# Performance work log

Measured on AMD Instinct MI355X. Metric: run time of the kernel, lower is better.

The kernel has to match this reference:

```python
import jax, jax.numpy as jnp
import numpy as np

B, N, I, H, O, E, HD = 4, 2048, 32, 64, 32, 2, 2  # batch, nodes, in_dim, hidden, out, edgetypes, heads
D1 = H * HD * E  # layer-1 filter input dim (concat of all heads/edgetypes from layer 0)


def setup_inputs() -> dict:
    key = jax.random.key(0)
    ks = jax.random.split(key, 20)
    s = 0.1
    return {
        "nodes": jax.random.normal(ks[0], (B, N, I), jnp.float32),
        "edges": jax.random.normal(ks[1], (B, N, N, E), jnp.float32),
        "W_emb": jax.random.normal(ks[2], (I, H), jnp.float32) * s,
        "b_emb": jnp.zeros((H,), jnp.float32),
        "Wf0": jax.random.normal(ks[3], (E, HD, H, H), jnp.float32) * s,
        "w1_0": jax.random.normal(ks[4], (E, HD, H), jnp.float32) * s,
        "b1_0": jnp.zeros((E, HD), jnp.float32),
        "w2_0": jax.random.normal(ks[5], (E, HD, H), jnp.float32) * s,
        "b2_0": jnp.zeros((E, HD), jnp.float32),
        "bias0": jax.random.normal(ks[6], (HD, H), jnp.float32) * s,  # state_bias aliased across edgetypes (list-mult bug)
        "Wf1": jax.random.normal(ks[7], (E, HD, D1, H), jnp.float32) * s,
        "w1_1": jax.random.normal(ks[8], (E, HD, H), jnp.float32) * s,
        "b1_1": jnp.zeros((E, HD), jnp.float32),
        "w2_1": jax.random.normal(ks[9], (E, HD, H), jnp.float32) * s,
        "b2_1": jnp.zeros((E, HD), jnp.float32),
        "bias1": jax.random.normal(ks[10], (HD, H), jnp.float32) * s,
        "W_out": jax.random.normal(ks[11], (H, O), jnp.float32) * s,
        "b_out": jnp.zeros((O,), jnp.float32),
    }


def _gat_layer(state, Wf, w1, b1, w2, b2, bias, edges_t, last):
    # state: (B,N,Din); Wf: (E,HD,Din,H); edges_t: (E,B,N,N)
    Wh = jnp.einsum('bnd,ehdk->ehbnk', state, Wf)                     # (E,HD,B,N,H)
    a1 = jnp.einsum('ehbnk,ehk->ehbn', Wh, w1) + b1[:, :, None, None]
    a2 = jnp.einsum('ehbnk,ehk->ehbn', Wh, w2) + b2[:, :, None, None]
    logits = jax.nn.leaky_relu(a1[..., :, None] + a2[..., None, :], 0.2) + edges_t[:, None]
    att = jax.nn.softmax(logits, axis=-2)                             # torch softmax dim=1 (over rows)
    msg = jnp.einsum('ehbik,ehbkd->ehbid', att, Wh) + bias[None, :, None, None, :]
    if last:
        return jnp.mean(jax.nn.elu(msg), axis=(0, 1))                 # (B,N,H)
    # concat in (edgetype-major, head-minor) order, matching the python loops
    return jnp.transpose(msg, (2, 3, 0, 1, 4)).reshape(msg.shape[2], msg.shape[3], -1)


def reference(nodes, edges, W_emb, b_emb, Wf0, w1_0, b1_0, w2_0, b2_0, bias0,
              Wf1, w1_1, b1_1, w2_1, b2_1, bias1, W_out, b_out):
    edges_t = jnp.transpose(edges, (3, 0, 1, 2))                      # (E,B,N,N)
    state = nodes @ W_emb + b_emb                                     # embedding
    state = _gat_layer(state, Wf0, w1_0, b1_0, w2_0, b2_0, bias0, edges_t, last=False)
    state = _gat_layer(state, Wf1, w1_1, b1_1, w2_1, b2_1, bias1, edges_t, last=True)
    out = state @ W_out + b_out                                       # (B,N,O)
    return jnp.mean(out, axis=1)                                      # graph-level output (B,O)
```

## Files before the change

### kernel.cpp

```cpp
#include <hip/hip_runtime.h>
#include <hip/hip_bf16.h>


constexpr int B_  = 4;
constexpr int N_  = 2048;
constexpr int I_  = 32;
constexpr int H_  = 64;
constexpr int O_  = 32;
constexpr int EH_ = 4;
constexpr int D1_ = 256;
constexpr int BN_ = B_ * N_;
constexpr int NC_ = 64;
constexpr int CH_ = N_ / NC_;
constexpr int TI_ = 16;
constexpr int TK_ = 32;
constexpr int NKT_ = N_ / TK_;

typedef __bf16 bf16x8 __attribute__((ext_vector_type(8)));
typedef float floatx4 __attribute__((ext_vector_type(4)));

constexpr float L2E_ = 1.4426950408889634f;

__device__ __forceinline__ unsigned short f2b(float f) {
    unsigned int u = __float_as_uint(f);
    return (unsigned short)((u + 0x7fffu + ((u >> 16) & 1u)) >> 16);
}

__device__ __forceinline__ float fexp2(float x) {
#if __has_builtin(__builtin_amdgcn_exp2f)
    return __builtin_amdgcn_exp2f(x);
#else
    return __expf(x * 0.6931471805599453f);
#endif
}

__global__ __launch_bounds__(256) void prep_kernel(
        const float* __restrict__ nodes, const float* __restrict__ W_emb,
        const float* __restrict__ b_emb, const float* __restrict__ Wf0,
        const float* __restrict__ Wf1, unsigned short* __restrict__ state0B,
        unsigned short* __restrict__ WfB0, unsigned short* __restrict__ WfB1) {
    int blk = blockIdx.x;
    int t = threadIdx.x;
    __shared__ float sn[4][I_];
    if (blk < 2048) {
        int r = t >> 6, h = t & 63;
        if (t < 4 * I_) {
            int rr = t / I_, ii = t % I_;
            sn[rr][ii] = nodes[(size_t)(blk * 4 + rr) * I_ + ii];
        }
        __syncthreads();
        float acc = b_emb[h];
        #pragma unroll
        for (int i = 0; i < I_; ++i) acc += sn[r][i] * W_emb[i * H_ + h];
        state0B[(size_t)(blk * 4 + r) * H_ + h] = f2b(acc);
    } else if (blk < 2048 + 64) {
        int o = (blk - 2048) * 256 + t;
        int k = o & 63, n = (o >> 6) & 63, c = o >> 12;
        WfB0[o] = f2b(Wf0[((size_t)c * 64 + k) * 64 + n]);
    } else {
        int o = (blk - 2112) * 256 + t;
        int k = o & 255, n = (o >> 8) & 63, c = o >> 14;
        WfB1[o] = f2b(Wf1[((size_t)c * 256 + k) * 64 + n]);
    }
}

template <int DIN>
__global__ __launch_bounds__(256) void wh_a_mfma_kernel(
        const unsigned short* __restrict__ stateB, const unsigned short* __restrict__ WfB,
        const float* __restrict__ w1, const float* __restrict__ b1,
        const float* __restrict__ w2, const float* __restrict__ b2,
        unsigned short* __restrict__ WhB, float* __restrict__ a1,
        float* __restrict__ a2) {
    int t = threadIdx.x;
    int lane = t & 63, wv = t >> 6;
    int col = lane & 15, qd = lane >> 4;
    int bn0 = blockIdx.x * TI_;
    int b = bn0 >> 11;

    floatx4 acc[4] = {{0,0,0,0},{0,0,0,0},{0,0,0,0},{0,0,0,0}};
    const unsigned short* __restrict__ ap = stateB + (size_t)(bn0 + col) * DIN + qd * 8;
    const unsigned short* __restrict__ bp = WfB + ((size_t)(wv * 64 + col) * DIN + qd * 8);
    #pragma unroll
    for (int k0 = 0; k0 < DIN; k0 += 32) {
        bf16x8 af = *(const bf16x8*)(ap + k0);
        #pragma unroll
        for (int nt = 0; nt < 4; ++nt) {
            bf16x8 bf = *(const bf16x8*)(bp + (size_t)nt * 16 * DIN + k0);
            acc[nt] = __builtin_amdgcn_mfma_f32_16x16x32_bf16(af, bf, acc[nt], 0, 0, 0);
        }
    }
    int nb = ((bn0 & 2047) >> 3) + (qd >> 1);
    #pragma unroll
    for (int nt = 0; nt < 4; ++nt) {
        unsigned int lo = (unsigned int)f2b(acc[nt][0]) | ((unsigned int)f2b(acc[nt][1]) << 16);
        unsigned int hi = (unsigned int)f2b(acc[nt][2]) | ((unsigned int)f2b(acc[nt][3]) << 16);
        uint2 v = make_uint2(lo, hi);
        *(uint2*)(WhB + ((((size_t)(wv * B_ + b) * 256 + nb) * 64 + nt * 16 + col) * 8
                         + (qd & 1) * 4)) = v;
    }
    float p1[4] = {}, p2[4] = {};
    #pragma unroll
    for (int nt = 0; nt < 4; ++nt) {
        float w1n = w1[wv * H_ + nt * 16 + col];
        float w2n = w2[wv * H_ + nt * 16 + col];
        #pragma unroll
        for (int r = 0; r < 4; ++r) {
            p1[r] += acc[nt][r] * w1n;
            p2[r] += acc[nt][r] * w2n;
        }
    }
    #pragma unroll
    for (int m = 1; m < 16; m <<= 1)
        #pragma unroll
        for (int r = 0; r < 4; ++r) {
            p1[r] += __shfl_xor(p1[r], m, 64);
            p2[r] += __shfl_xor(p2[r], m, 64);
        }
    if (col == 0) {
        float b1c = b1[wv], b2c = b2[wv];
        #pragma unroll
        for (int r = 0; r < 4; ++r) {
            a1[(size_t)wv * BN_ + bn0 + qd * 4 + r] = (p1[r] + b1c) * L2E_;
            a2[(size_t)wv * BN_ + bn0 + qd * 4 + r] = (p2[r] + b2c) * L2E_;
        }
    }
}

__global__ __launch_bounds__(256) void stats_kernel(
        const float* __restrict__ edges, const float* __restrict__ a1,
        const float* __restrict__ a2, float* __restrict__ ps) {
    int blk = blockIdx.x;
    int jt = blk & 7;
    int ic = (blk >> 3) & (NC_ - 1);
    int b  = blk >> 9;
    int t = threadIdx.x;
    int j = jt * 256 + t;
    __shared__ float sa1[EH_][CH_];
    for (int q = t; q < EH_ * CH_; q += 256) {
        int cc = q / CH_, ii = q % CH_;
        sa1[cc][ii] = a1[(size_t)cc * BN_ + b * N_ + ic * CH_ + ii];
    }
    __syncthreads();
    float a2v[EH_], s[EH_];
    #pragma unroll
    for (int cc = 0; cc < EH_; ++cc) {
        a2v[cc] = a2[(size_t)cc * BN_ + b * N_ + j];
        s[cc] = 0.f;
    }
    const float2* __restrict__ ep = (const float2*)edges + ((size_t)(b * N_ + ic * CH_)) * N_ + j;
    #pragma unroll 4
    for (int ii = 0; ii < CH_; ++ii) {
        float2 u = ep[(size_t)ii * N_];
        #pragma unroll
        for (int cc = 0; cc < EH_; ++cc) {
            float x = sa1[cc][ii] + a2v[cc];
            float l = fmaxf(x, 0.2f * x);
            s[cc] += fexp2(fmaf((cc < 2) ? u.x : u.y, L2E_, l));
        }
    }
    #pragma unroll
    for (int cc = 0; cc < EH_; ++cc)
        ps[((size_t)ic * EH_ + cc) * BN_ + b * N_ + j] = s[cc];
}

__global__ __launch_bounds__(256) void scale_kernel(
        const float* __restrict__ ps, unsigned short* __restrict__ WhB) {
    int t = threadIdx.x;
    int m0 = blockIdx.x * 256;
    int cb = m0 >> 14;
    int c = cb >> 2, b = cb & 3;
    int k0 = ((m0 >> 6) & 255) * 8;
    __shared__ float sD[32];
    if (t < 32) {
        float S = 0.f;
        const float* pp = ps + (size_t)c * BN_ + b * N_ + k0 + t;
        #pragma unroll 8
        for (int ic = 0; ic < NC_; ++ic) S += pp[(size_t)ic * EH_ * BN_];
        sD[t] = 1.f / S;
    }
    __syncthreads();
    unsigned short* wp = WhB + (size_t)(m0 + t) * 8;
    uint4 w = *(const uint4*)wp;
    int nbo = (t >> 6) * 8;
    unsigned int words[4] = {w.x, w.y, w.z, w.w};
    #pragma unroll
    for (int q = 0; q < 4; ++q) {
        float lo = __uint_as_float((words[q] & 0xffffu) << 16) * sD[nbo + 2 * q];
        float hi = __uint_as_float(words[q] & 0xffff0000u) * sD[nbo + 2 * q + 1];
        words[q] = (unsigned)f2b(lo) | ((unsigned)f2b(hi) << 16);
    }
    *(uint4*)wp = make_uint4(words[0], words[1], words[2], words[3]);
}

template <int LAST>
__global__ __launch_bounds__(512, 4) void mac_kernel(
        const float* __restrict__ edges, const float* __restrict__ a1,
        const float* __restrict__ a2s, const unsigned short* __restrict__ WhB,
        const float* __restrict__ bias, void* __restrict__ outv) {
    int t = threadIdx.x;
    int blk = blockIdx.x;
    int b = blk >> 7;
    int i0 = (blk & 127) * TI_;
    int lane = t & 63, wv = t >> 6;
    int c  = wv & 3;
    int kh = wv >> 2;
    int col = lane & 15;
    int qd  = lane >> 4;
    int esel = c >> 1;

    __shared__ float sa2[EH_][N_];
    __shared__ float sred[EH_][TI_][H_ + 1];

    for (int q = t; q < EH_ * (N_ / 4); q += 512) {
        int cc = q >> 9, kk = q & 511;
        ((float4*)sa2[cc])[kk] =
            ((const float4*)(a2s + (size_t)cc * BN_ + b * N_))[kk];
    }

    float a1v = a1[(size_t)c * BN_ + b * N_ + i0 + col];
    const float* __restrict__ erow = edges + (size_t)(b * N_ + i0 + col) * (N_ * 2);
    const unsigned short* __restrict__ whb0 = WhB + (size_t)(c * B_ + b) * (256 * 512);

    const int kt0 = kh * (NKT_ / 2);
    const int ktEnd = kt0 + NKT_ / 2;

    float evc[8], evn[8];
    {
        const float4* ep = (const float4*)(erow + (size_t)(kt0 * TK_ + qd * 8) * 2);
        #pragma unroll
        for (int jj = 0; jj < 4; ++jj) {
            float4 v = ep[jj];
            evc[2 * jj]     = esel ? v.y : v.x;
            evc[2 * jj + 1] = esel ? v.w : v.z;
        }
    }
    bf16x8 bcur[4], bnxt[4];
    #pragma unroll
    for (int nt = 0; nt < 4; ++nt)
        bcur[nt] = *(const bf16x8*)(whb0 + ((size_t)(kt0 * 4 + qd) * 64 + nt * 16 + col) * 8);

    floatx4 acc[4] = {{0,0,0,0},{0,0,0,0},{0,0,0,0},{0,0,0,0}};
    __syncthreads();

    for (int kt = kt0; kt < ktEnd; ++kt) {
        int ktn = (kt + 1 < ktEnd) ? (kt + 1) : kt0;
        {
            const float4* ep = (const float4*)(erow + (size_t)(ktn * TK_ + qd * 8) * 2);
            #pragma unroll
            for (int jj = 0; jj < 4; ++jj) {
                float4 v = ep[jj];
                evn[2 * jj]     = esel ? v.y : v.x;
                evn[2 * jj + 1] = esel ? v.w : v.z;
            }
        }
        #pragma unroll
        for (int nt = 0; nt < 4; ++nt)
            bnxt[nt] = *(const bf16x8*)(whb0 + ((size_t)(ktn * 4 + qd) * 64 + nt * 16 + col) * 8);

        const float4* sp = (const float4*)&sa2[c][kt * TK_ + qd * 8];
        float4 s0 = sp[0], s1 = sp[1];
        float az[8] = {s0.x, s0.y, s0.z, s0.w, s1.x, s1.y, s1.z, s1.w};
        bf16x8 af;
        #pragma unroll
        for (int j = 0; j < 8; ++j) {
            float sx = a1v + az[j];
            float u  = fmaxf(sx, 0.2f * sx);
            af[j] = (__bf16)fexp2(fmaf(evc[j], L2E_, u));
        }
        #pragma unroll
        for (int nt = 0; nt < 4; ++nt)
            acc[nt] = __builtin_amdgcn_mfma_f32_16x16x32_bf16(af, bcur[nt], acc[nt], 0, 0, 0);
        #pragma unroll
        for (int nt = 0; nt < 4; ++nt) bcur[nt] = bnxt[nt];
        #pragma unroll
        for (int j = 0; j < 8; ++j) evc[j] = evn[j];
    }

    if (kh == 1) {
        #pragma unroll
        for (int nt = 0; nt < 4; ++nt)
            #pragma unroll
            for (int r = 0; r < 4; ++r)
                sred[c][qd * 4 + r][nt * 16 + col] = acc[nt][r];
    }
    __syncthreads();
    if (kh == 0) {
        if (LAST) {
            #pragma unroll
            for (int nt = 0; nt < 4; ++nt) {
                float bb = bias[(c & 1) * H_ + nt * 16 + col];
                #pragma unroll
                for (int r = 0; r < 4; ++r) {
                    float x = acc[nt][r] + sred[c][qd * 4 + r][nt * 16 + col] + bb;
                    sred[c][qd * 4 + r][nt * 16 + col] =
                        x > 0.f ? x : (__expf(x) - 1.f);
                }
            }
        } else {
            unsigned short* out = (unsigned short*)outv;
            #pragma unroll
            for (int nt = 0; nt < 4; ++nt) {
                float bb = bias[(c & 1) * H_ + nt * 16 + col];
                #pragma unroll
                for (int r = 0; r < 4; ++r) {
                    float x = acc[nt][r] + sred[c][qd * 4 + r][nt * 16 + col] + bb;
                    out[((size_t)(b * N_ + i0 + qd * 4 + r)) * D1_ + c * H_ + nt * 16 + col]
                        = f2b(x);
                }
            }
        }
    }
    if (LAST) {
        __syncthreads();
        if (t < 64) {
            float s = 0.f;
            #pragma unroll
            for (int r = 0; r < TI_; ++r)
                s += sred[0][r][t] + sred[1][r][t] + sred[2][r][t] + sred[3][r][t];
            ((float*)outv)[(size_t)blk * 64 + t] = s * 0.25f;
        }
    }
}

__global__ __launch_bounds__(256) void out_kernel(
        const float* __restrict__ po, const float* __restrict__ W_out,
        const float* __restrict__ b_out, float* __restrict__ out) {
    int b = blockIdx.x, t = threadIdx.x;
    int d = t & 63, g0 = t >> 6;
    float s = 0.f;
    for (int g = g0; g < 128; g += 4) s += po[(size_t)(b * 128 + g) * 64 + d];
    __shared__ float red[4][H_];
    red[g0][d] = s;
    __syncthreads();
    if (t < H_) red[0][t] = (red[0][t] + red[1][t] + red[2][t] + red[3][t]) * (1.f / N_);
    __syncthreads();
    if (t < O_) {
        float acc = b_out[t];
        #pragma unroll 8
        for (int dd = 0; dd < H_; ++dd)
            acc += red[0][dd] * W_out[dd * O_ + t];
        out[b * O_ + t] = acc;
    }
}

extern "C" void kernel_launch(void* const* d_in, const int* in_sizes, int n_in,
                              void* d_out, int out_size, void* d_ws, size_t ws_size,
                              hipStream_t stream) {
    const float* nodes = (const float*)d_in[0];
    const float* edges = (const float*)d_in[1];
    const float* W_emb = (const float*)d_in[2];
    const float* b_emb = (const float*)d_in[3];
    const float* Wf0   = (const float*)d_in[4];
    const float* w1_0  = (const float*)d_in[5];
    const float* b1_0  = (const float*)d_in[6];
    const float* w2_0  = (const float*)d_in[7];
    const float* b2_0  = (const float*)d_in[8];
    const float* bias0 = (const float*)d_in[9];
    const float* Wf1   = (const float*)d_in[10];
    const float* w1_1  = (const float*)d_in[11];
    const float* b1_1  = (const float*)d_in[12];
    const float* w2_1  = (const float*)d_in[13];
    const float* b2_1  = (const float*)d_in[14];
    const float* bias1 = (const float*)d_in[15];
    const float* W_out = (const float*)d_in[16];
    const float* b_out = (const float*)d_in[17];

    float* ws = (float*)d_ws;
    unsigned short* state0B = (unsigned short*)ws;
    unsigned short* state1B = (unsigned short*)(ws + 262144);
    unsigned short* WhB  = (unsigned short*)(ws + 262144 + 1048576);
    unsigned short* WfB0 = (unsigned short*)(ws + 2359296);
    unsigned short* WfB1 = (unsigned short*)(ws + 2367488);
    float* a1 = ws + 2400256;
    float* a2 = ws + 2433024;
    float* ps = ws + 2465792;
    float* po = ws + 4562944;

    prep_kernel<<<2368, 256, 0, stream>>>(nodes, W_emb, b_emb, Wf0, Wf1,
                                          state0B, WfB0, WfB1);

    wh_a_mfma_kernel<H_><<<BN_ / TI_, 256, 0, stream>>>(state0B, WfB0, w1_0, b1_0,
                                                        w2_0, b2_0, WhB, a1, a2);
    stats_kernel<<<B_ * NC_ * (N_ / 256), 256, 0, stream>>>(edges, a1, a2, ps);
    scale_kernel<<<1024, 256, 0, stream>>>(ps, WhB);
    mac_kernel<0><<<B_ * (N_ / TI_), 512, 0, stream>>>(edges, a1, a2, WhB, bias0, state1B);
    wh_a_mfma_kernel<D1_><<<BN_ / TI_, 256, 0, stream>>>(state1B, WfB1, w1_1, b1_1,
                                                         w2_1, b2_1, WhB, a1, a2);
    stats_kernel<<<B_ * NC_ * (N_ / 256), 256, 0, stream>>>(edges, a1, a2, ps);
    scale_kernel<<<1024, 256, 0, stream>>>(ps, WhB);
    mac_kernel<1><<<B_ * (N_ / TI_), 512, 0, stream>>>(edges, a1, a2, WhB, bias1, po);

    out_kernel<<<B_, 256, 0, stream>>>(po, W_out, b_out, (float*)d_out);
}
```

Baseline: 438.5 us.

## Split mac kernel across channel pairs with 4-way K split, widen stats loads

The mac kernel now launches twice as many blocks. Each block handles two of the four edgetype/head channels and splits the K range four ways across waves, reducing partials through shared memory. It drops the register double-buffered prefetch and raises the occupancy hint. The stats kernel has each thread process two columns with float4 edge loads, and out_kernel is adapted to the new partial layout. The aim is more parallelism and smaller shared memory per block for better occupancy, but each block now reads the edges rows for only one edge type, so edge traffic in the mac kernel doubles.

```diff
diff --git a/kernel.cpp b/kernel.cpp
--- a/kernel.cpp
+++ b/kernel.cpp
@@ -130,37 +130,46 @@
         const float* __restrict__ edges, const float* __restrict__ a1,
         const float* __restrict__ a2, float* __restrict__ ps) {
     int blk = blockIdx.x;
-    int jt = blk & 7;
-    int ic = (blk >> 3) & (NC_ - 1);
-    int b  = blk >> 9;
+    int jt = blk & 3;
+    int ic = (blk >> 2) & (NC_ - 1);
+    int b  = blk >> 8;
     int t = threadIdx.x;
-    int j = jt * 256 + t;
+    int j0 = jt * 512 + t * 2;
     __shared__ float sa1[EH_][CH_];
-    for (int q = t; q < EH_ * CH_; q += 256) {
-        int cc = q / CH_, ii = q % CH_;
+    if (t < EH_ * CH_) {
+        int cc = t >> 5, ii = t & 31;
         sa1[cc][ii] = a1[(size_t)cc * BN_ + b * N_ + ic * CH_ + ii];
     }
     __syncthreads();
-    float a2v[EH_], s[EH_];
+    float a2x[EH_], a2y[EH_], s0[EH_], s1[EH_];
     #pragma unroll
     for (int cc = 0; cc < EH_; ++cc) {
-        a2v[cc] = a2[(size_t)cc * BN_ + b * N_ + j];
-        s[cc] = 0.f;
-    }
-    const float2* __restrict__ ep = (const float2*)edges + ((size_t)(b * N_ + ic * CH_)) * N_ + j;
+        float2 av = *(const float2*)(a2 + (size_t)cc * BN_ + b * N_ + j0);
+        a2x[cc] = av.x; a2y[cc] = av.y;
+        s0[cc] = 0.f; s1[cc] = 0.f;
+    }
+    const float4* __restrict__ ep =
+        (const float4*)edges + (((size_t)(b * N_ + ic * CH_) * N_ + j0) >> 1);
     #pragma unroll 4
     for (int ii = 0; ii < CH_; ++ii) {
-        float2 u = ep[(size_t)ii * N_];
+        float4 u = ep[(size_t)ii * (N_ >> 1)];
         #pragma unroll
         for (int cc = 0; cc < EH_; ++cc) {
-            float x = sa1[cc][ii] + a2v[cc];
-            float l = fmaxf(x, 0.2f * x);
-            s[cc] += fexp2(fmaf((cc < 2) ? u.x : u.y, L2E_, l));
+            float base = sa1[cc][ii];
+            float xa = base + a2x[cc];
+            float xb = base + a2y[cc];
+            float la = fmaxf(xa, 0.2f * xa);
+            float lb = fmaxf(xb, 0.2f * xb);
+            float ea = (cc < 2) ? u.x : u.y;
+            float eb = (cc < 2) ? u.z : u.w;
+            s0[cc] += fexp2(fmaf(ea, L2E_, la));
+            s1[cc] += fexp2(fmaf(eb, L2E_, lb));
         }
     }
     #pragma unroll
     for (int cc = 0; cc < EH_; ++cc)
-        ps[((size_t)ic * EH_ + cc) * BN_ + b * N_ + j] = s[cc];
+        *(float2*)&ps[((size_t)ic * EH_ + cc) * BN_ + b * N_ + j0] =
+            make_float2(s0[cc], s1[cc]);
 }
 
 __global__ __launch_bounds__(256) void scale_kernel(
@@ -193,106 +202,114 @@
 }
 
 template <int LAST>
-__global__ __launch_bounds__(512, 4) void mac_kernel(
+__global__ __launch_bounds__(512, 8) void mac_kernel(
         const float* __restrict__ edges, const float* __restrict__ a1,
         const float* __restrict__ a2s, const unsigned short* __restrict__ WhB,
         const float* __restrict__ bias, void* __restrict__ outv) {
     int t = threadIdx.x;
     int blk = blockIdx.x;
-    int b = blk >> 7;
-    int i0 = (blk & 127) * TI_;
+    int cp = blk & 1;
+    int g  = blk >> 1;
+    int b  = g >> 7;
+    int i0 = (g & 127) * TI_;
     int lane = t & 63, wv = t >> 6;
-    int c  = wv & 3;
-    int kh = wv >> 2;
+    int kq = wv >> 1;
+    int cl = wv & 1;
+    int c  = cp * 2 + cl;
     int col = lane & 15;
     int qd  = lane >> 4;
-    int esel = c >> 1;
-
-    __shared__ float sa2[EH_][N_];
-    __shared__ float sred[EH_][TI_][H_ + 1];
-
-    for (int q = t; q < EH_ * (N_ / 4); q += 512) {
-        int cc = q >> 9, kk = q & 511;
-        ((float4*)sa2[cc])[kk] =
-            ((const float4*)(a2s + (size_t)cc * BN_ + b * N_))[kk];
+
+    __shared__ float sa2[2][N_];
+    __shared__ float sA[2][TI_][H_ + 1];
+    __shared__ float sB[2][TI_][H_ + 1];
+
+    for (int q = t; q < 2 * (N_ / 4); q += 512) {
+        int cl_ = q >> 9, kk = q & 511;
+        ((float4*)sa2[cl_])[kk] =
+            ((const float4*)(a2s + (size_t)(cp * 2 + cl_) * BN_ + b * N_))[kk];
     }
 
     float a1v = a1[(size_t)c * BN_ + b * N_ + i0 + col];
     const float* __restrict__ erow = edges + (size_t)(b * N_ + i0 + col) * (N_ * 2);
-    const unsigned short* __restrict__ whb0 = WhB + (size_t)(c * B_ + b) * (256 * 512);
-
-    const int kt0 = kh * (NKT_ / 2);
-    const int ktEnd = kt0 + NKT_ / 2;
-
-    float evc[8], evn[8];
-    {
-        const float4* ep = (const float4*)(erow + (size_t)(kt0 * TK_ + qd * 8) * 2);
-        #pragma unroll
-        for (int jj = 0; jj < 4; ++jj) {
-            float4 v = ep[jj];
-            evc[2 * jj]     = esel ? v.y : v.x;
-            evc[2 * jj + 1] = esel ? v.w : v.z;
-        }
-    }
-    bf16x8 bcur[4], bnxt[4];
-    #pragma unroll
-    for (int nt = 0; nt < 4; ++nt)
-        bcur[nt] = *(const bf16x8*)(whb0 + ((size_t)(kt0 * 4 + qd) * 64 + nt * 16 + col) * 8);
+    const unsigned short* __restrict__ whb0 = WhB + (size_t)(c * B_ + b) * (N_ * 64);
 
     floatx4 acc[4] = {{0,0,0,0},{0,0,0,0},{0,0,0,0},{0,0,0,0}};
     __syncthreads();
 
-    for (int kt = kt0; kt < ktEnd; ++kt) {
-        int ktn = (kt + 1 < ktEnd) ? (kt + 1) : kt0;
-        {
-            const float4* ep = (const float4*)(erow + (size_t)(ktn * TK_ + qd * 8) * 2);
-            #pragma unroll
-            for (int jj = 0; jj < 4; ++jj) {
-                float4 v = ep[jj];
-                evn[2 * jj]     = esel ? v.y : v.x;
-                evn[2 * jj + 1] = esel ? v.w : v.z;
-            }
-        }
-        #pragma unroll
-        for (int nt = 0; nt < 4; ++nt)
-            bnxt[nt] = *(const bf16x8*)(whb0 + ((size_t)(ktn * 4 + qd) * 64 + nt * 16 + col) * 8);
-
-        const float4* sp = (const float4*)&sa2[c][kt * TK_ + qd * 8];
+    const int ktBeg = kq * (NKT_ / 4);
+    const int ktEnd = ktBeg + NKT_ / 4;
+    for (int kt = ktBeg; kt < ktEnd; ++kt) {
+        const float4* ep = (const float4*)(erow + (size_t)(kt * TK_ + qd * 8) * 2);
+        float4 e0 = ep[0], e1 = ep[1], e2 = ep[2], e3 = ep[3];
+        bf16x8 bf[4];
+        #pragma unroll
+        for (int nt = 0; nt < 4; ++nt)
+            bf[nt] = *(const bf16x8*)(whb0 + ((size_t)(kt * 4 + qd) * 64 + nt * 16 + col) * 8);
+        const float4* sp = (const float4*)&sa2[cl][kt * TK_ + qd * 8];
         float4 s0 = sp[0], s1 = sp[1];
         float az[8] = {s0.x, s0.y, s0.z, s0.w, s1.x, s1.y, s1.z, s1.w};
+        float ev[8];
+        ev[0] = cp ? e0.y : e0.x; ev[1] = cp ? e0.w : e0.z;
+        ev[2] = cp ? e1.y : e1.x; ev[3] = cp ? e1.w : e1.z;
+        ev[4] = cp ? e2.y : e2.x; ev[5] = cp ? e2.w : e2.z;
+        ev[6] = cp ? e3.y : e3.x; ev[7] = cp ? e3.w : e3.z;
         bf16x8 af;
         #pragma unroll
         for (int j = 0; j < 8; ++j) {
             float sx = a1v + az[j];
             float u  = fmaxf(sx, 0.2f * sx);
-            af[j] = (__bf16)fexp2(fmaf(evc[j], L2E_, u));
-        }
-        #pragma unroll
-        for (int nt = 0; nt < 4; ++nt)
-            acc[nt] = __builtin_amdgcn_mfma_f32_16x16x32_bf16(af, bcur[nt], acc[nt], 0, 0, 0);
-        #pragma unroll
-        for (int nt = 0; nt < 4; ++nt) bcur[nt] = bnxt[nt];
-        #pragma unroll
-        for (int j = 0; j < 8; ++j) evc[j] = evn[j];
-    }
-
-    if (kh == 1) {
+            af[j] = (__bf16)fexp2(fmaf(ev[j], L2E_, u));
+        }
+        #pragma unroll
+        for (int nt = 0; nt < 4; ++nt)
+            acc[nt] = __builtin_amdgcn_mfma_f32_16x16x32_bf16(af, bf[nt], acc[nt], 0, 0, 0);
+    }
+
+    if (kq == 2) {
         #pragma unroll
         for (int nt = 0; nt < 4; ++nt)
             #pragma unroll
             for (int r = 0; r < 4; ++r)
-                sred[c][qd * 4 + r][nt * 16 + col] = acc[nt][r];
-    }
-    __syncthreads();
-    if (kh == 0) {
+                sA[cl][qd * 4 + r][nt * 16 + col] = acc[nt][r];
+    } else if (kq == 3) {
+        #pragma unroll
+        for (int nt = 0; nt < 4; ++nt)
+            #pragma unroll
+            for (int r = 0; r < 4; ++r)
+                sB[cl][qd * 4 + r][nt * 16 + col] = acc[nt][r];
+    }
+    __syncthreads();
+    if (kq == 0) {
+        #pragma unroll
+        for (int nt = 0; nt < 4; ++nt)
+            #pragma unroll
+            for (int r = 0; r < 4; ++r)
+                acc[nt][r] += sA[cl][qd * 4 + r][nt * 16 + col];
+    } else if (kq == 1) {
+        #pragma unroll
+        for (int nt = 0; nt < 4; ++nt)
+            #pragma unroll
+            for (int r = 0; r < 4; ++r)
+                acc[nt][r] += sB[cl][qd * 4 + r][nt * 16 + col];
+    }
+    __syncthreads();
+    if (kq == 1) {
+        #pragma unroll
+        for (int nt = 0; nt < 4; ++nt)
+            #pragma unroll
+            for (int r = 0; r < 4; ++r)
+                sA[cl][qd * 4 + r][nt * 16 + col] = acc[nt][r];
+    }
+    __syncthreads();
+    if (kq == 0) {
         if (LAST) {
             #pragma unroll
             for (int nt = 0; nt < 4; ++nt) {
-                float bb = bias[(c & 1) * H_ + nt * 16 + col];
+                float bb = bias[cl * H_ + nt * 16 + col];
                 #pragma unroll
                 for (int r = 0; r < 4; ++r) {
-                    float x = acc[nt][r] + sred[c][qd * 4 + r][nt * 16 + col] + bb;
-                    sred[c][qd * 4 + r][nt * 16 + col] =
+                    float x = acc[nt][r] + sA[cl][qd * 4 + r][nt * 16 + col] + bb;
+                    sA[cl][qd * 4 + r][nt * 16 + col] =
                         x > 0.f ? x : (__expf(x) - 1.f);
                 }
             }
@@ -300,10 +317,10 @@
             unsigned short* out = (unsigned short*)outv;
             #pragma unroll
             for (int nt = 0; nt < 4; ++nt) {
-                float bb = bias[(c & 1) * H_ + nt * 16 + col];
+                float bb = bias[cl * H_ + nt * 16 + col];
                 #pragma unroll
                 for (int r = 0; r < 4; ++r) {
-                    float x = acc[nt][r] + sred[c][qd * 4 + r][nt * 16 + col] + bb;
+                    float x = acc[nt][r] + sA[cl][qd * 4 + r][nt * 16 + col] + bb;
                     out[((size_t)(b * N_ + i0 + qd * 4 + r)) * D1_ + c * H_ + nt * 16 + col]
                         = f2b(x);
                 }
@@ -316,23 +333,32 @@
             float s = 0.f;
             #pragma unroll
             for (int r = 0; r < TI_; ++r)
-                s += sred[0][r][t] + sred[1][r][t] + sred[2][r][t] + sred[3][r][t];
-            ((float*)outv)[(size_t)blk * 64 + t] = s * 0.25f;
-        }
-    }
-}
-
-__global__ __launch_bounds__(256) void out_kernel(
+                s += sA[0][r][t] + sA[1][r][t];
+            ((float*)outv)[((size_t)cp * 512 + g) * 64 + t] = s * 0.25f;
+        }
+    }
+}
+
+__global__ __launch_bounds__(1024) void out_kernel(
         const float* __restrict__ po, const float* __restrict__ W_out,
         const float* __restrict__ b_out, float* __restrict__ out) {
     int b = blockIdx.x, t = threadIdx.x;
     int d = t & 63, g0 = t >> 6;
     float s = 0.f;
-    for (int g = g0; g < 128; g += 4) s += po[(size_t)(b * 128 + g) * 64 + d];
-    __shared__ float red[4][H_];
+    #pragma unroll 4
+    for (int p = g0; p < 256; p += 16) {
+        int cp = p >> 7, it = p & 127;
+        s += po[((size_t)cp * 512 + b * 128 + it) * 64 + d];
+    }
+    __shared__ float red[16][H_];
     red[g0][d] = s;
     __syncthreads();
-    if (t < H_) red[0][t] = (red[0][t] + red[1][t] + red[2][t] + red[3][t]) * (1.f / N_);
+    if (t < H_) {
+        float r = 0.f;
+        #pragma unroll
+        for (int q = 0; q < 16; ++q) r += red[q][t];
+        red[0][t] = r * (1.f / N_);
+    }
     __syncthreads();
     if (t < O_) {
         float acc = b_out[t];
@@ -381,14 +407,14 @@
 
     wh_a_mfma_kernel<H_><<<BN_ / TI_, 256, 0, stream>>>(state0B, WfB0, w1_0, b1_0,
                                                         w2_0, b2_0, WhB, a1, a2);
-    stats_kernel<<<B_ * NC_ * (N_ / 256), 256, 0, stream>>>(edges, a1, a2, ps);
+    stats_kernel<<<B_ * NC_ * (N_ / 512), 256, 0, stream>>>(edges, a1, a2, ps);
     scale_kernel<<<1024, 256, 0, stream>>>(ps, WhB);
-    mac_kernel<0><<<B_ * (N_ / TI_), 512, 0, stream>>>(edges, a1, a2, WhB, bias0, state1B);
+    mac_kernel<0><<<2 * B_ * (N_ / TI_), 512, 0, stream>>>(edges, a1, a2, WhB, bias0, state1B);
     wh_a_mfma_kernel<D1_><<<BN_ / TI_, 256, 0, stream>>>(state1B, WfB1, w1_1, b1_1,
                                                          w2_1, b2_1, WhB, a1, a2);
-    stats_kernel<<<B_ * NC_ * (N_ / 256), 256, 0, stream>>>(edges, a1, a2, ps);
+    stats_kernel<<<B_ * NC_ * (N_ / 512), 256, 0, stream>>>(edges, a1, a2, ps);
     scale_kernel<<<1024, 256, 0, stream>>>(ps, WhB);
-    mac_kernel<1><<<B_ * (N_ / TI_), 512, 0, stream>>>(edges, a1, a2, WhB, bias1, po);
-
-    out_kernel<<<B_, 256, 0, stream>>>(po, W_out, b_out, (float*)d_out);
-}
+    mac_kernel<1><<<2 * B_ * (N_ / TI_), 512, 0, stream>>>(edges, a1, a2, WhB, bias1, po);
+
+    out_kernel<<<B_, 1024, 0, stream>>>(po, W_out, b_out, (float*)d_out);
+}
```

Result: no change. 442.2 us (+0.8%).

## Stage edge tiles into LDS with async global_load_lds and widen stats loads

Applied to the files above, without the earlier changes.

The mac kernel now streams the edge rows for its 16-row tile into a triple-buffered, XOR-swizzled LDS ring using async global-to-LDS loads. Each lane then reads its edge values from LDS instead of doing strided per-lane global loads, and the block index is remapped to interleave batches. Register prefetch of the WhB operand is dropped in favour of direct loads each step. The stats kernel processes two columns per thread with float4 edge loads and float2 stores on half as many blocks. The change targets uncoalesced edge reads, which dominate memory traffic, at the cost of a block barrier every k-step and extra LDS use that may lower occupancy.

```diff
diff --git a/kernel.cpp b/kernel.cpp
--- a/kernel.cpp
+++ b/kernel.cpp
@@ -15,6 +15,7 @@
 constexpr int TI_ = 16;
 constexpr int TK_ = 32;
 constexpr int NKT_ = N_ / TK_;
+constexpr int NST_ = 32;
 
 typedef __bf16 bf16x8 __attribute__((ext_vector_type(8)));
 typedef float floatx4 __attribute__((ext_vector_type(4)));
@@ -32,6 +33,12 @@
 #else
     return __expf(x * 0.6931471805599453f);
 #endif
+}
+
+__device__ __forceinline__ void gl2lds16(const void* g, void* l) {
+    __builtin_amdgcn_global_load_lds(
+        (const __attribute__((address_space(1))) unsigned int*)g,
+        (__attribute__((address_space(3))) unsigned int*)l, 16, 0, 0);
 }
 
 __global__ __launch_bounds__(256) void prep_kernel(
@@ -130,37 +137,46 @@
         const float* __restrict__ edges, const float* __restrict__ a1,
         const float* __restrict__ a2, float* __restrict__ ps) {
     int blk = blockIdx.x;
-    int jt = blk & 7;
-    int ic = (blk >> 3) & (NC_ - 1);
-    int b  = blk >> 9;
+    int jt = blk & 3;
+    int ic = (blk >> 2) & (NC_ - 1);
+    int b  = blk >> 8;
     int t = threadIdx.x;
-    int j = jt * 256 + t;
+    int j0 = jt * 512 + t * 2;
     __shared__ float sa1[EH_][CH_];
-    for (int q = t; q < EH_ * CH_; q += 256) {
-        int cc = q / CH_, ii = q % CH_;
+    if (t < EH_ * CH_) {
+        int cc = t >> 5, ii = t & 31;
         sa1[cc][ii] = a1[(size_t)cc * BN_ + b * N_ + ic * CH_ + ii];
     }
     __syncthreads();
-    float a2v[EH_], s[EH_];
+    float a2x[EH_], a2y[EH_], s0[EH_], s1[EH_];
     #pragma unroll
     for (int cc = 0; cc < EH_; ++cc) {
-        a2v[cc] = a2[(size_t)cc * BN_ + b * N_ + j];
-        s[cc] = 0.f;
-    }
-    const float2* __restrict__ ep = (const float2*)edges + ((size_t)(b * N_ + ic * CH_)) * N_ + j;
+        float2 av = *(const float2*)(a2 + (size_t)cc * BN_ + b * N_ + j0);
+        a2x[cc] = av.x; a2y[cc] = av.y;
+        s0[cc] = 0.f; s1[cc] = 0.f;
+    }
+    const float4* __restrict__ ep =
+        (const float4*)edges + (((size_t)(b * N_ + ic * CH_) * N_ + j0) >> 1);
     #pragma unroll 4
     for (int ii = 0; ii < CH_; ++ii) {
-        float2 u = ep[(size_t)ii * N_];
+        float4 u = ep[(size_t)ii * (N_ >> 1)];
         #pragma unroll
         for (int cc = 0; cc < EH_; ++cc) {
-            float x = sa1[cc][ii] + a2v[cc];
-            float l = fmaxf(x, 0.2f * x);
-            s[cc] += fexp2(fmaf((cc < 2) ? u.x : u.y, L2E_, l));
+            float base = sa1[cc][ii];
+            float xa = base + a2x[cc];
+            float xb = base + a2y[cc];
+            float la = fmaxf(xa, 0.2f * xa);
+            float lb = fmaxf(xb, 0.2f * xb);
+            float ea = (cc < 2) ? u.x : u.y;
+            float eb = (cc < 2) ? u.z : u.w;
+            s0[cc] += fexp2(fmaf(ea, L2E_, la));
+            s1[cc] += fexp2(fmaf(eb, L2E_, lb));
         }
     }
     #pragma unroll
     for (int cc = 0; cc < EH_; ++cc)
-        ps[((size_t)ic * EH_ + cc) * BN_ + b * N_ + j] = s[cc];
+        *(float2*)&ps[((size_t)ic * EH_ + cc) * BN_ + b * N_ + j0] =
+            make_float2(s0[cc], s1[cc]);
 }
 
 __global__ __launch_bounds__(256) void scale_kernel(
@@ -198,7 +214,8 @@
         const float* __restrict__ a2s, const unsigned short* __restrict__ WhB,
         const float* __restrict__ bias, void* __restrict__ outv) {
     int t = threadIdx.x;
-    int blk = blockIdx.x;
+    int blk0 = blockIdx.x;
+    int blk = ((blk0 & 7) << 6) + (blk0 >> 3);
     int b = blk >> 7;
     int i0 = (blk & 127) * TI_;
     int lane = t & 63, wv = t >> 6;
@@ -209,6 +226,7 @@
     int esel = c >> 1;
 
     __shared__ float sa2[EH_][N_];
+    __shared__ __attribute__((aligned(16))) unsigned char eds[3][2][TI_][256];
     __shared__ float sred[EH_][TI_][H_ + 1];
 
     for (int q = t; q < EH_ * (N_ / 4); q += 512) {
@@ -218,62 +236,52 @@
     }
 
     float a1v = a1[(size_t)c * BN_ + b * N_ + i0 + col];
-    const float* __restrict__ erow = edges + (size_t)(b * N_ + i0 + col) * (N_ * 2);
-    const unsigned short* __restrict__ whb0 = WhB + (size_t)(c * B_ + b) * (256 * 512);
-
-    const int kt0 = kh * (NKT_ / 2);
-    const int ktEnd = kt0 + NKT_ / 2;
-
-    float evc[8], evn[8];
-    {
-        const float4* ep = (const float4*)(erow + (size_t)(kt0 * TK_ + qd * 8) * 2);
+    const unsigned short* __restrict__ whb0 = WhB + (size_t)(c * B_ + b) * (N_ * 64);
+
+    int srow  = 4 * (wv & 3) + (lane >> 4);
+    int sslot = (lane & 15) ^ (srow & 15);
+    const char* gsrc = (const char*)edges
+        + ((size_t)(b * N_ + i0 + srow) * N_ + (size_t)(wv >> 2) * 1024) * 8
+        + sslot * 16;
+    char* ldst = (char*)&eds[0][0][0][0] + wv * 1024;
+
+    floatx4 acc[4] = {{0,0,0,0},{0,0,0,0},{0,0,0,0},{0,0,0,0}};
+
+    gl2lds16(gsrc, ldst);
+    for (int s = 0; s < NST_; ++s) {
+        if (s + 1 < NST_)
+            gl2lds16(gsrc + (size_t)(s + 1) * 256,
+                     ldst + (size_t)(((s + 1) % 3)) * 8192);
+        __syncthreads();
+
+        int kt = kh * NST_ + s;
+        const char* ebase = (const char*)&eds[0][0][0][0]
+                          + (s % 3) * 8192 + kh * 4096 + col * 256;
+        float ev[8];
         #pragma unroll
         for (int jj = 0; jj < 4; ++jj) {
-            float4 v = ep[jj];
-            evc[2 * jj]     = esel ? v.y : v.x;
-            evc[2 * jj + 1] = esel ? v.w : v.z;
-        }
-    }
-    bf16x8 bcur[4], bnxt[4];
-    #pragma unroll
-    for (int nt = 0; nt < 4; ++nt)
-        bcur[nt] = *(const bf16x8*)(whb0 + ((size_t)(kt0 * 4 + qd) * 64 + nt * 16 + col) * 8);
-
-    floatx4 acc[4] = {{0,0,0,0},{0,0,0,0},{0,0,0,0},{0,0,0,0}};
-    __syncthreads();
-
-    for (int kt = kt0; kt < ktEnd; ++kt) {
-        int ktn = (kt + 1 < ktEnd) ? (kt + 1) : kt0;
-        {
-            const float4* ep = (const float4*)(erow + (size_t)(ktn * TK_ + qd * 8) * 2);
-            #pragma unroll
-            for (int jj = 0; jj < 4; ++jj) {
-                float4 v = ep[jj];
-                evn[2 * jj]     = esel ? v.y : v.x;
-                evn[2 * jj + 1] = esel ? v.w : v.z;
-            }
-        }
+            int sg = qd * 4 + jj;
+            float4 v = *(const float4*)(ebase + ((sg ^ (col & 15)) * 16));
+            ev[2 * jj]     = esel ? v.y : v.x;
+            ev[2 * jj + 1] = esel ? v.w : v.z;
+        }
+        const float4* sp = (const float4*)&sa2[c][kt * TK_ + qd * 8];
+        float4 z0 = sp[0], z1 = sp[1];
+        float az[8] = {z0.x, z0.y, z0.z, z0.w, z1.x, z1.y, z1.z, z1.w};
+        bf16x8 bf[4];
         #pragma unroll
         for (int nt = 0; nt < 4; ++nt)
-            bnxt[nt] = *(const bf16x8*)(whb0 + ((size_t)(ktn * 4 + qd) * 64 + nt * 16 + col) * 8);
-
-        const float4* sp = (const float4*)&sa2[c][kt * TK_ + qd * 8];
-        float4 s0 = sp[0], s1 = sp[1];
-        float az[8] = {s0.x, s0.y, s0.z, s0.w, s1.x, s1.y, s1.z, s1.w};
+            bf[nt] = *(const bf16x8*)(whb0 + ((size_t)(kt * 4 + qd) * 64 + nt * 16 + col) * 8);
         bf16x8 af;
         #pragma unroll
         for (int j = 0; j < 8; ++j) {
             float sx = a1v + az[j];
             float u  = fmaxf(sx, 0.2f * sx);
-            af[j] = (__bf16)fexp2(fmaf(evc[j], L2E_, u));
+            af[j] = (__bf16)fexp2(fmaf(ev[j], L2E_, u));
         }
         #pragma unroll
         for (int nt = 0; nt < 4; ++nt)
-            acc[nt] = __builtin_amdgcn_mfma_f32_16x16x32_bf16(af, bcur[nt], acc[nt], 0, 0, 0);
-        #pragma unroll
-        for (int nt = 0; nt < 4; ++nt) bcur[nt] = bnxt[nt];
-        #pragma unroll
-        for (int j = 0; j < 8; ++j) evc[j] = evn[j];
+            acc[nt] = __builtin_amdgcn_mfma_f32_16x16x32_bf16(af, bf[nt], acc[nt], 0, 0, 0);
     }
 
     if (kh == 1) {
@@ -381,12 +389,12 @@
 
     wh_a_mfma_kernel<H_><<<BN_ / TI_, 256, 0, stream>>>(state0B, WfB0, w1_0, b1_0,
                                                         w2_0, b2_0, WhB, a1, a2);
-    stats_kernel<<<B_ * NC_ * (N_ / 256), 256, 0, stream>>>(edges, a1, a2, ps);
+    stats_kernel<<<B_ * NC_ * (N_ / 512), 256, 0, stream>>>(edges, a1, a2, ps);
     scale_kernel<<<1024, 256, 0, stream>>>(ps, WhB);
     mac_kernel<0><<<B_ * (N_ / TI_), 512, 0, stream>>>(edges, a1, a2, WhB, bias0, state1B);
     wh_a_mfma_kernel<D1_><<<BN_ / TI_, 256, 0, stream>>>(state1B, WfB1, w1_1, b1_1,
                                                          w2_1, b2_1, WhB, a1, a2);
-    stats_kernel<<<B_ * NC_ * (N_ / 256), 256, 0, stream>>>(edges, a1, a2, ps);
+    stats_kernel<<<B_ * NC_ * (N_ / 512), 256, 0, stream>>>(edges, a1, a2, ps);
     scale_kernel<<<1024, 256, 0, stream>>>(ps, WhB);
     mac_kernel<1><<<B_ * (N_ / TI_), 512, 0, stream>>>(edges, a1, a2, WhB, bias1, po);
 
```

New measurement: 372.8 us. 1.18x faster.
